# Kernel optimization log

Hardware: AMD Instinct MI355X
Metric: run time of the kernel (lower is better)

Reference implementation:

```python
import jax, jax.numpy as jnp
import numpy as np

B, L, H = 16, 2048, 1024
N = B * L
K_SEL = 8192
LN_EPS = 1e-12
PD_EPS = 1e-6  # torch f.pairwise_distance default eps


def setup_inputs() -> dict:
    key = jax.random.key(0)
    k1, k2, k3, k4 = jax.random.split(key, 4)
    msp = jax.random.normal(k1, (B, L, H), dtype=jnp.float32)
    lab = jax.random.normal(k2, (B, L, H), dtype=jnp.float32)
    # mask with exactly K_SEL true positions (static compaction size)
    perm = jax.random.permutation(k3, N)[:K_SEL]
    mask = jnp.zeros((N,), dtype=bool).at[perm].set(True).reshape(B, L)
    dense_w = jax.random.normal(k4, (H, H), dtype=jnp.float32) / np.sqrt(H)
    return {
        "masked_sentence_prediction": msp,
        "label_embeddings": lab,
        "label_mask": mask,
        "dense_w": dense_w,
        "dense_b": jnp.zeros((H,), dtype=jnp.float32),
        "ln_gamma": jnp.ones((H,), dtype=jnp.float32),
        "ln_beta": jnp.zeros((H,), dtype=jnp.float32),
        "K": K_SEL,
    }


def reference(masked_sentence_prediction, label_embeddings, label_mask,
              dense_w, dense_b, ln_gamma, ln_beta, K):
    Hd = masked_sentence_prediction.shape[-1]
    mask_flat = label_mask.reshape(-1)
    # stream compaction: rows where mask is true (static size K)
    idx = jnp.nonzero(mask_flat, size=K)[0]
    preds = masked_sentence_prediction.reshape(-1, Hd)[idx]      # [K, H]
    labels = label_embeddings.reshape(-1, Hd)[idx]               # [K, H]
    # dense + LayerNorm
    h = preds @ dense_w.T + dense_b
    mu = jnp.mean(h, axis=-1, keepdims=True)
    var = jnp.mean(jnp.square(h - mu), axis=-1, keepdims=True)
    h = (h - mu) * jax.lax.rsqrt(var + LN_EPS) * ln_gamma + ln_beta
    # contrastive logits against dynamic sentence vocabulary
    logits = h @ labels.T                                        # [K, K]
    log_probs = jax.nn.log_softmax(logits, axis=1)
    probs = jnp.exp(log_probs)
    eye = jnp.eye(K, dtype=logits.dtype)
    per_example_loss_distance = jnp.sum(jnp.abs(probs - eye + PD_EPS), axis=1)
    per_example_loss_product = -jnp.diagonal(log_probs)
    denom = K + 1e-5
    loss_distance = jnp.sum(per_example_loss_distance) / denom
    loss_product = jnp.sum(per_example_loss_product) / denom
    loss_variance_distance = jnp.var(per_example_loss_distance, ddof=1)
    loss_variance_product = jnp.var(per_example_loss_product, ddof=1)
    return (logits, per_example_loss_distance, per_example_loss_product,
            loss_distance, loss_product, loss_variance_distance, loss_variance_product)
```

## Files before the change

### kernel.cpp

```cpp
#include <hip/hip_runtime.h>
#include <cstdint>

#define NROWS 32768
#define HD    1024
#define KSEL  8192
#define LN_EPS 1e-12f
#define PD_EPS 1e-6f

typedef unsigned short u16;
typedef __bf16 bf16x8 __attribute__((ext_vector_type(8)));
typedef float  f32x4  __attribute__((ext_vector_type(4)));

__device__ inline u16 f2bf(float f) {
    union { float f; uint32_t u; } x; x.f = f;
    uint32_t r = (x.u + 0x7fffu + ((x.u >> 16) & 1u)) >> 16;
    return (u16)r;
}

__device__ inline uint2 pack4(float a, float b, float c, float d) {
    uint2 r;
    r.x = (uint32_t)f2bf(a) | ((uint32_t)f2bf(b) << 16);
    r.y = (uint32_t)f2bf(c) | ((uint32_t)f2bf(d) << 16);
    return r;
}

__global__ void compact_mask_k(const uint8_t* mb, const int32_t* mi, int* idx) {
    __shared__ int cnt[1024];
    __shared__ int tmp[1024];
    __shared__ int mode_s;
    const int t = threadIdx.x;
    const int per = NROWS / 1024;
    const int base = t * per;
    int c0 = 0;
    for (int i = 0; i < per; ++i) c0 += (mb[base + i] != 0);
    tmp[t] = c0;
    __syncthreads();
    for (int off = 512; off > 0; off >>= 1) {
        if (t < off) tmp[t] += tmp[t + off];
        __syncthreads();
    }
    if (t == 0) mode_s = (tmp[0] == KSEL) ? 0 : 1;
    __syncthreads();
    const int mode = mode_s;
    int c = c0;
    if (mode) { c = 0; for (int i = 0; i < per; ++i) c += (mi[base + i] != 0); }
    cnt[t] = c;
    __syncthreads();
    for (int off = 1; off < 1024; off <<= 1) {
        int add = (t >= off) ? cnt[t - off] : 0;
        __syncthreads();
        cnt[t] += add;
        __syncthreads();
    }
    int pos = cnt[t] - c;
    for (int i = 0; i < per; ++i) {
        bool v = mode ? (mi[base + i] != 0) : (mb[base + i] != 0);
        if (v) idx[pos++] = base + i;
    }
}

__global__ void gather_conv_k(const float* __restrict__ msp, const float* __restrict__ lab,
                              const int* __restrict__ idx, const float* __restrict__ W,
                              u16* __restrict__ predsB, u16* __restrict__ labelsB,
                              u16* __restrict__ Wb) {
    const int b = blockIdx.x;
    const int t = threadIdx.x;
    if (b < KSEL) {
        const int src = idx[b];
        float4 p = *(const float4*)(msp + (size_t)src * HD + t * 4);
        float4 q = *(const float4*)(lab + (size_t)src * HD + t * 4);
        *(uint2*)(predsB  + (size_t)b * HD + t * 4) = pack4(p.x, p.y, p.z, p.w);
        *(uint2*)(labelsB + (size_t)b * HD + t * 4) = pack4(q.x, q.y, q.z, q.w);
    } else {
        const int i = ((b - KSEL) * 256 + t) * 4;
        float4 v = *(const float4*)(W + i);
        *(uint2*)(Wb + i) = pack4(v.x, v.y, v.z, v.w);
    }
}

#define STAGE(XPTR, ROWBASE, KT, I, LBASE) do {                                      \
    const int f_ = (I) * 512 + tid;                                                  \
    const int r_ = f_ >> 3;                                                          \
    const int sp_ = (f_ & 7) ^ (r_ & 7);                                             \
    const u16* g_ = (XPTR) + (size_t)((ROWBASE) + r_) * Kd + koff + (KT) * 64 + sp_ * 8; \
    __builtin_amdgcn_global_load_lds(                                                \
        (const __attribute__((address_space(1))) void*)g_,                           \
        (__attribute__((address_space(3))) void*)(lds + (LBASE) + f_ * 8), 16, 0, 0);\
} while (0)

#define GEMM_PRO_AND_KLOOP(TVAL)                                                      \
    const int nx  = N >> 8;                                                           \
    int wg  = ((nwg & 7) == 0) ? ((bid & 7) * (nwg >> 3) + (bid >> 3)) : bid;         \
    const int bm = wg / nx, bn = wg % nx;                                             \
    const size_t brow = (size_t)bm << 8, bcol = (size_t)bn << 8;                      \
    const int tid = threadIdx.x;                                                      \
    const int l = tid & 63, wid = tid >> 6;                                           \
    const int wm = wid >> 2, wn = wid & 3;                                            \
    const int lr = l & 15, lq = l >> 4;                                               \
    const int sw = lr & 7;                                                            \
    f32x4 acc[8][4] = {};                                                             \
    const int arow = (wm * 128 + lr) * 64;                                            \
    const int brow2 = (wn * 64 + lr) * 64;                                            \
    const int s0 = (lq ^ sw) * 8;                                                     \
    const int s1 = ((4 + lq) ^ sw) * 8;                                               \
    _Pragma("unroll")                                                                 \
    for (int i = 0; i < 4; ++i) STAGE(A,  brow, 0, i, 0);                             \
    _Pragma("unroll")                                                                 \
    for (int i = 0; i < 4; ++i) STAGE(Bt, bcol, 0, i, 49152);                         \
    _Pragma("unroll")                                                                 \
    for (int i = 0; i < 4; ++i) STAGE(A,  brow, 1, i, 16384);                         \
    asm volatile("s_waitcnt vmcnt(4)" ::: "memory");                                  \
    __builtin_amdgcn_s_barrier();                                                     \
    const int T = (TVAL);                                                             \
    int abi = 0;                                                                      \
    _Pragma("unroll 1")                                                               \
    for (int t = 0; t < T; ++t) {                                                     \
        const int aB = abi * 16384;                                                   \
        const int bB = 49152 + (t & 1) * 16384;                                       \
        const int aN = (abi >= 1 ? abi - 1 : 2) * 16384;                              \
        const int bN = 49152 + ((t + 1) & 1) * 16384;                                 \
        bf16x8 a0[8], b0[4], a1[8], b1[4];                                            \
                     \
        _Pragma("unroll")                                                             \
        for (int mi = 0; mi < 8; ++mi)                                                \
            a0[mi] = *(const bf16x8*)(lds + aB + arow + mi * 1024 + s0);              \
        _Pragma("unroll")                                                             \
        for (int ni = 0; ni < 4; ++ni)                                                \
            b0[ni] = *(const bf16x8*)(lds + bB + brow2 + ni * 1024 + s0);             \
        _Pragma("unroll")                                                             \
        for (int mi = 0; mi < 8; ++mi)                                                \
            a1[mi] = *(const bf16x8*)(lds + aB + arow + mi * 1024 + s1);              \
        _Pragma("unroll")                                                             \
        for (int ni = 0; ni < 4; ++ni)                                                \
            b1[ni] = *(const bf16x8*)(lds + bB + brow2 + ni * 1024 + s1);             \
                      \
        if (t + 1 < T) {                                                              \
            STAGE(Bt, bcol, t + 1, 0, bN); STAGE(Bt, bcol, t + 1, 1, bN);             \
            STAGE(Bt, bcol, t + 1, 2, bN); STAGE(Bt, bcol, t + 1, 3, bN);             \
        }                                                                             \
        if (t + 2 < T) {                                                              \
            STAGE(A, brow, t + 2, 0, aN); STAGE(A, brow, t + 2, 1, aN);               \
            STAGE(A, brow, t + 2, 2, aN); STAGE(A, brow, t + 2, 3, aN);               \
        }                                                                             \
                     \
        _Pragma("unroll")                                                             \
        for (int mi = 0; mi < 8; ++mi) {                                              \
            _Pragma("unroll")                                                         \
            for (int ni = 0; ni < 4; ++ni)                                            \
                acc[mi][ni] = __builtin_amdgcn_mfma_f32_16x16x32_bf16(a0[mi], b0[ni], acc[mi][ni], 0, 0, 0); \
        }                                                                             \
        _Pragma("unroll")                                                             \
        for (int mi = 0; mi < 8; ++mi) {                                              \
            _Pragma("unroll")                                                         \
            for (int ni = 0; ni < 4; ++ni)                                            \
                acc[mi][ni] = __builtin_amdgcn_mfma_f32_16x16x32_bf16(a1[mi], b1[ni], acc[mi][ni], 0, 0, 0); \
        }                                                                             \
                      \
        if (t < T - 2) { asm volatile("s_waitcnt vmcnt(4)" ::: "memory"); }           \
        else           { asm volatile("s_waitcnt vmcnt(0)" ::: "memory"); }           \
        __builtin_amdgcn_s_barrier();                                                 \
        abi = (abi == 2) ? 0 : abi + 1;                                               \
    }

__global__ __launch_bounds__(512, 2)
void gemm256a_k(const u16* __restrict__ A, const u16* __restrict__ Bt,
                float* __restrict__ C, int M, int N, int Kd) {
    extern __shared__ u16 lds[];
    const int nwg = (M >> 8) * (N >> 8);
    int bid = blockIdx.x;
    const int half = (bid >= nwg) ? 1 : 0;
    if (half) bid -= nwg;
    const int KdH = Kd >> 1;
    const int koff = half * KdH;
    float* Cp = C + (size_t)half * ((size_t)M * N);
    GEMM_PRO_AND_KLOOP(KdH >> 6);
    #pragma unroll
    for (int m = 0; m < 8; ++m) {
        const size_t rb = brow + wm * 128 + m * 16 + lq * 4;
        #pragma unroll
        for (int n = 0; n < 4; ++n) {
            const size_t cb = bcol + wn * 64 + n * 16 + lr;
            #pragma unroll
            for (int rr = 0; rr < 4; ++rr)
                Cp[(rb + rr) * (size_t)N + cb] = acc[m][n][rr];
        }
    }
}

__global__ __launch_bounds__(512, 2)
void gemm256s_k(const u16* __restrict__ A, const u16* __restrict__ Bt,
                float* __restrict__ C, int M, int N, int Kd,
                float2* __restrict__ pst) {
    extern __shared__ u16 lds[];
    const int nwg = (M >> 8) * (N >> 8);
    int bid = blockIdx.x;
    const int koff = 0;
    GEMM_PRO_AND_KLOOP(Kd >> 6);

    float2* sbuf = (float2*)lds;
    #pragma unroll
    for (int m = 0; m < 8; ++m) {
        #pragma unroll
        for (int rr = 0; rr < 4; ++rr) {
            float v0 = acc[m][0][rr], v1 = acc[m][1][rr];
            float v2 = acc[m][2][rr], v3 = acc[m][3][rr];
            float mx = fmaxf(fmaxf(v0, v1), fmaxf(v2, v3));
            #pragma unroll
            for (int o = 1; o < 16; o <<= 1) mx = fmaxf(mx, __shfl_xor(mx, o));
            float se = __expf(v0 - mx) + __expf(v1 - mx) + __expf(v2 - mx) + __expf(v3 - mx);
            #pragma unroll
            for (int o = 1; o < 16; o <<= 1) se += __shfl_xor(se, o);
            if (lr == 0) {
                const int rl = wm * 128 + m * 16 + lq * 4 + rr;
                sbuf[rl * 5 + wn] = make_float2(mx, se);
            }
        }
        const size_t rb = brow + wm * 128 + m * 16 + lq * 4;
        #pragma unroll
        for (int n = 0; n < 4; ++n) {
            const size_t cb = bcol + wn * 64 + n * 16 + lr;
            #pragma unroll
            for (int rr = 0; rr < 4; ++rr)
                __builtin_nontemporal_store(acc[m][n][rr], &C[(rb + rr) * (size_t)N + cb]);
        }
    }
    asm volatile("s_waitcnt lgkmcnt(0)" ::: "memory");
    __builtin_amdgcn_s_barrier();
    if (tid < 256) {
        const float2 p0 = sbuf[tid * 5 + 0], p1 = sbuf[tid * 5 + 1];
        const float2 p2 = sbuf[tid * 5 + 2], p3 = sbuf[tid * 5 + 3];
        const float M2 = fmaxf(fmaxf(p0.x, p1.x), fmaxf(p2.x, p3.x));
        const float S2 = p0.y * __expf(p0.x - M2) + p1.y * __expf(p1.x - M2)
                       + p2.y * __expf(p2.x - M2) + p3.y * __expf(p3.x - M2);
        pst[(brow + tid) * (N >> 8) + bn] = make_float2(M2, S2);
    }
}

__global__ __launch_bounds__(256)
void loss_final_k(const float2* __restrict__ pst, const float* __restrict__ logits,
                  float* __restrict__ peld, float* __restrict__ pelp) {
    const int tid = threadIdx.x;
    const int wv = tid >> 6, half = (tid & 63) >> 5, l5 = tid & 31;
    const int row = blockIdx.x * 8 + wv * 2 + half;
    const float2 p = pst[(size_t)row * 32 + l5];
    const float d = logits[(size_t)row * (KSEL + 1)];
    float M = p.x;
    #pragma unroll
    for (int o = 1; o < 32; o <<= 1) M = fmaxf(M, __shfl_xor(M, o));
    float S = p.y * __expf(p.x - M);
    #pragma unroll
    for (int o = 1; o < 32; o <<= 1) S += __shfl_xor(S, o);
    if (l5 == 0) {
        const float pi = __expf(d - M) / S;
        peld[row] = 2.0f - 2.0f * pi + (float)(KSEL - 2) * PD_EPS;
        pelp[row] = M + __logf(S) - d;
    }
}

__device__ inline float blockSum(float v, float* red) {
    #pragma unroll
    for (int o = 32; o > 0; o >>= 1) v += __shfl_down(v, o);
    __syncthreads();
    if ((threadIdx.x & 63) == 0) red[threadIdx.x >> 6] = v;
    __syncthreads();
    return red[0] + red[1] + red[2] + red[3];
}

__global__ void ln_k(const float* __restrict__ Hp0, const float* __restrict__ Hp1,
                     const float* __restrict__ bias,
                     const float* __restrict__ gamma, const float* __restrict__ beta,
                     u16* __restrict__ Hb) {
    __shared__ float red[4];
    const int r = blockIdx.x, t = threadIdx.x;
    float4 x4 = *(const float4*)(Hp0 + (size_t)r * HD + t * 4);
    float4 y4 = *(const float4*)(Hp1 + (size_t)r * HD + t * 4);
    float4 b4 = *(const float4*)(bias + t * 4);
    float x[4] = { x4.x + y4.x + b4.x, x4.y + y4.y + b4.y,
                   x4.z + y4.z + b4.z, x4.w + y4.w + b4.w };
    float s = x[0] + x[1] + x[2] + x[3];
    float mu = blockSum(s, red) * (1.0f / HD);
    float d0 = x[0] - mu, d1 = x[1] - mu, d2 = x[2] - mu, d3 = x[3] - mu;
    float vs = d0 * d0 + d1 * d1 + d2 * d2 + d3 * d3;
    float var = blockSum(vs, red) * (1.0f / HD);
    float rs = rsqrtf(var + LN_EPS);
    float4 g4 = *(const float4*)(gamma + t * 4);
    float4 e4 = *(const float4*)(beta + t * 4);
    float y0 = d0 * rs * g4.x + e4.x;
    float y1 = d1 * rs * g4.y + e4.y;
    float y2 = d2 * rs * g4.z + e4.z;
    float y3 = d3 * rs * g4.w + e4.w;
    *(uint2*)(Hb + (size_t)r * HD + t * 4) = pack4(y0, y1, y2, y3);
}

__global__ __launch_bounds__(1024)
void reduce_k(const float* __restrict__ peld, const float* __restrict__ pelp,
              float* __restrict__ scalars) {
    __shared__ double red[4][16];
    const int t = threadIdx.x;
    double a = 0.0, b = 0.0, c = 0.0, d = 0.0;
    for (int i = t; i < KSEL; i += 1024) {
        const double pd = (double)peld[i];
        const double pp = (double)pelp[i];
        a += pd; b += pd * pd; c += pp; d += pp * pp;
    }
    #pragma unroll
    for (int o = 32; o > 0; o >>= 1) {
        a += __shfl_down(a, o); b += __shfl_down(b, o);
        c += __shfl_down(c, o); d += __shfl_down(d, o);
    }
    const int wv = t >> 6;
    if ((t & 63) == 0) { red[0][wv] = a; red[1][wv] = b; red[2][wv] = c; red[3][wv] = d; }
    __syncthreads();
    if (t == 0) {
        double s1 = 0, s2 = 0, s3 = 0, s4 = 0;
        #pragma unroll
        for (int i = 0; i < 16; ++i) { s1 += red[0][i]; s2 += red[1][i]; s3 += red[2][i]; s4 += red[3][i]; }
        const double Kd = (double)KSEL;
        const double denom = Kd + 1e-5;
        scalars[0] = (float)(s1 / denom);
        scalars[1] = (float)(s3 / denom);
        scalars[2] = (float)((s2 - s1 * s1 / Kd) / (Kd - 1.0));
        scalars[3] = (float)((s4 - s3 * s3 / Kd) / (Kd - 1.0));
    }
}

extern "C" void kernel_launch(void* const* d_in, const int* in_sizes, int n_in,
                              void* d_out, int out_size, void* d_ws, size_t ws_size,
                              hipStream_t stream) {
    const float* msp   = (const float*)d_in[0];
    const float* lab   = (const float*)d_in[1];
    const void*  mask  = d_in[2];
    const float* W     = (const float*)d_in[3];
    const float* bias  = (const float*)d_in[4];
    const float* gamma = (const float*)d_in[5];
    const float* beta  = (const float*)d_in[6];
    float* out = (float*)d_out;
    char*  ws  = (char*)d_ws;

    int*    idx     = (int*)ws;
    float2* pst     = (float2*)(ws + 65536);
    u16*    wBf     = (u16*)(ws + 65536);
    u16*    labelsB = (u16*)(ws + (size_t)(4  << 20));
    u16*    hB      = (u16*)(ws + (size_t)(20 << 20));
    u16*    predsB  = (u16*)d_out;
    float*  hPre    = out + ((size_t)8 << 20);

    float* peld    = out + (size_t)KSEL * KSEL;
    float* pelp    = peld + KSEL;
    float* scalars = pelp + KSEL;

    hipFuncSetAttribute(reinterpret_cast<const void*>(&gemm256a_k),
                        hipFuncAttributeMaxDynamicSharedMemorySize, 163840);
    hipFuncSetAttribute(reinterpret_cast<const void*>(&gemm256s_k),
                        hipFuncAttributeMaxDynamicSharedMemorySize, 163840);

    compact_mask_k<<<1, 1024, 0, stream>>>((const uint8_t*)mask, (const int32_t*)mask, idx);
    gather_conv_k<<<KSEL + 1024, 256, 0, stream>>>(msp, lab, idx, W, predsB, labelsB, wBf);
    gemm256a_k<<<2 * (KSEL / 256) * (HD / 256), 512, 163840, stream>>>(
        predsB, wBf, hPre, KSEL, HD, HD);
    ln_k<<<KSEL, 256, 0, stream>>>(hPre, hPre + (size_t)KSEL * HD, bias, gamma, beta, hB);
    gemm256s_k<<<(KSEL / 256) * (KSEL / 256), 512, 163840, stream>>>(
        hB, labelsB, out, KSEL, KSEL, HD, pst);
    loss_final_k<<<KSEL / 8, 256, 0, stream>>>(pst, out, peld, pelp);
    reduce_k<<<1, 1024, 0, stream>>>(peld, pelp, scalars);
}
```

Measured before the change: 267.2 us.

## Switch GEMM inner loop from 16x16x32 to 32x32x16 bf16 MFMA

Replaces the 16x16x32 MFMA tiling with 32x32x16 MFMA instructions. Each wave now computes 4x2 tiles of 32x32 instead of 8x4 tiles of 16x16, which changes the LDS fragment reads, the swizzle offsets and the epilogue row/column mapping. The aim is fewer MFMA issues and LDS reads per unit of work and higher matrix-core throughput. The softmax-stats epilogue now reduces across 32 lanes, and the logits store in that kernel becomes a regular store instead of a nontemporal one, which may change cache behaviour for the large logits write.

```diff
diff --git a/kernel.cpp b/kernel.cpp
--- a/kernel.cpp
+++ b/kernel.cpp
@@ -9,7 +9,7 @@
 
 typedef unsigned short u16;
 typedef __bf16 bf16x8 __attribute__((ext_vector_type(8)));
-typedef float  f32x4  __attribute__((ext_vector_type(4)));
+typedef float  f32x16 __attribute__((ext_vector_type(16)));
 
 __device__ inline u16 f2bf(float f) {
     union { float f; uint32_t u; } x; x.f = f;
@@ -96,13 +96,16 @@
     const int tid = threadIdx.x;                                                      \
     const int l = tid & 63, wid = tid >> 6;                                           \
     const int wm = wid >> 2, wn = wid & 3;                                            \
-    const int lr = l & 15, lq = l >> 4;                                               \
-    const int sw = lr & 7;                                                            \
-    f32x4 acc[8][4] = {};                                                             \
-    const int arow = (wm * 128 + lr) * 64;                                            \
-    const int brow2 = (wn * 64 + lr) * 64;                                            \
-    const int s0 = (lq ^ sw) * 8;                                                     \
-    const int s1 = ((4 + lq) ^ sw) * 8;                                               \
+    const int r5 = l & 31, hk = l >> 5;                                               \
+    const int sw = l & 7;                                                             \
+    f32x16 acc[4][2] = {};                                                            \
+    const int arow = (wm * 128 + r5) * 64;                                            \
+    const int brow2 = (wn * 64 + r5) * 64;                                            \
+                              \
+    const int s0 = ((0 + hk) ^ sw) * 8;                                               \
+    const int s1 = ((2 + hk) ^ sw) * 8;                                               \
+    const int s2 = ((4 + hk) ^ sw) * 8;                                               \
+    const int s3 = ((6 + hk) ^ sw) * 8;                                               \
     _Pragma("unroll")                                                                 \
     for (int i = 0; i < 4; ++i) STAGE(A,  brow, 0, i, 0);                             \
     _Pragma("unroll")                                                                 \
@@ -119,20 +122,22 @@
         const int bB = 49152 + (t & 1) * 16384;                                       \
         const int aN = (abi >= 1 ? abi - 1 : 2) * 16384;                              \
         const int bN = 49152 + ((t + 1) & 1) * 16384;                                 \
-        bf16x8 a0[8], b0[4], a1[8], b1[4];                                            \
-                     \
+        bf16x8 a[4][4], b[4][2];                                                      \
+                                           \
         _Pragma("unroll")                                                             \
-        for (int mi = 0; mi < 8; ++mi)                                                \
-            a0[mi] = *(const bf16x8*)(lds + aB + arow + mi * 1024 + s0);              \
+        for (int mi = 0; mi < 4; ++mi) {                                              \
+            a[0][mi] = *(const bf16x8*)(lds + aB + arow + mi * 2048 + s0);            \
+            a[1][mi] = *(const bf16x8*)(lds + aB + arow + mi * 2048 + s1);            \
+            a[2][mi] = *(const bf16x8*)(lds + aB + arow + mi * 2048 + s2);            \
+            a[3][mi] = *(const bf16x8*)(lds + aB + arow + mi * 2048 + s3);            \
+        }                                                                             \
         _Pragma("unroll")                                                             \
-        for (int ni = 0; ni < 4; ++ni)                                                \
-            b0[ni] = *(const bf16x8*)(lds + bB + brow2 + ni * 1024 + s0);             \
-        _Pragma("unroll")                                                             \
-        for (int mi = 0; mi < 8; ++mi)                                                \
-            a1[mi] = *(const bf16x8*)(lds + aB + arow + mi * 1024 + s1);              \
-        _Pragma("unroll")                                                             \
-        for (int ni = 0; ni < 4; ++ni)                                                \
-            b1[ni] = *(const bf16x8*)(lds + bB + brow2 + ni * 1024 + s1);             \
+        for (int ni = 0; ni < 2; ++ni) {                                              \
+            b[0][ni] = *(const bf16x8*)(lds + bB + brow2 + ni * 2048 + s0);           \
+            b[1][ni] = *(const bf16x8*)(lds + bB + brow2 + ni * 2048 + s1);           \
+            b[2][ni] = *(const bf16x8*)(lds + bB + brow2 + ni * 2048 + s2);           \
+            b[3][ni] = *(const bf16x8*)(lds + bB + brow2 + ni * 2048 + s3);           \
+        }                                                                             \
                       \
         if (t + 1 < T) {                                                              \
             STAGE(Bt, bcol, t + 1, 0, bN); STAGE(Bt, bcol, t + 1, 1, bN);             \
@@ -142,20 +147,17 @@
             STAGE(A, brow, t + 2, 0, aN); STAGE(A, brow, t + 2, 1, aN);               \
             STAGE(A, brow, t + 2, 2, aN); STAGE(A, brow, t + 2, 3, aN);               \
         }                                                                             \
-                     \
+              \
         _Pragma("unroll")                                                             \
-        for (int mi = 0; mi < 8; ++mi) {                                              \
+        for (int kk = 0; kk < 4; ++kk) {                                              \
             _Pragma("unroll")                                                         \
-            for (int ni = 0; ni < 4; ++ni)                                            \
-                acc[mi][ni] = __builtin_amdgcn_mfma_f32_16x16x32_bf16(a0[mi], b0[ni], acc[mi][ni], 0, 0, 0); \
-        }                                                                             \
-        _Pragma("unroll")                                                             \
-        for (int mi = 0; mi < 8; ++mi) {                                              \
-            _Pragma("unroll")                                                         \
-            for (int ni = 0; ni < 4; ++ni)                                            \
-                acc[mi][ni] = __builtin_amdgcn_mfma_f32_16x16x32_bf16(a1[mi], b1[ni], acc[mi][ni], 0, 0, 0); \
-        }                                                                             \
-                      \
+            for (int mi = 0; mi < 4; ++mi) {                                          \
+                _Pragma("unroll")                                                     \
+                for (int ni = 0; ni < 2; ++ni)                                        \
+                    acc[mi][ni] = __builtin_amdgcn_mfma_f32_32x32x16_bf16(            \
+                        a[kk][mi], b[kk][ni], acc[mi][ni], 0, 0, 0);                  \
+            }                                                                         \
+        }                                                                             \
         if (t < T - 2) { asm volatile("s_waitcnt vmcnt(4)" ::: "memory"); }           \
         else           { asm volatile("s_waitcnt vmcnt(0)" ::: "memory"); }           \
         __builtin_amdgcn_s_barrier();                                                 \
@@ -175,14 +177,16 @@
     float* Cp = C + (size_t)half * ((size_t)M * N);
     GEMM_PRO_AND_KLOOP(KdH >> 6);
     #pragma unroll
-    for (int m = 0; m < 8; ++m) {
-        const size_t rb = brow + wm * 128 + m * 16 + lq * 4;
+    for (int mi = 0; mi < 4; ++mi) {
         #pragma unroll
-        for (int n = 0; n < 4; ++n) {
-            const size_t cb = bcol + wn * 64 + n * 16 + lr;
+        for (int ni = 0; ni < 2; ++ni) {
+            const size_t cb = bcol + wn * 64 + ni * 32 + r5;
             #pragma unroll
-            for (int rr = 0; rr < 4; ++rr)
-                Cp[(rb + rr) * (size_t)N + cb] = acc[m][n][rr];
+            for (int reg = 0; reg < 16; ++reg) {
+                const size_t rb = brow + wm * 128 + mi * 32
+                                + (reg & 3) + 8 * (reg >> 2) + 4 * hk;
+                Cp[rb * (size_t)N + cb] = acc[mi][ni][reg];
+            }
         }
     }
 }
@@ -199,29 +203,30 @@
 
     float2* sbuf = (float2*)lds;
     #pragma unroll
-    for (int m = 0; m < 8; ++m) {
+    for (int mi = 0; mi < 4; ++mi) {
         #pragma unroll
-        for (int rr = 0; rr < 4; ++rr) {
-            float v0 = acc[m][0][rr], v1 = acc[m][1][rr];
-            float v2 = acc[m][2][rr], v3 = acc[m][3][rr];
-            float mx = fmaxf(fmaxf(v0, v1), fmaxf(v2, v3));
+        for (int reg = 0; reg < 16; ++reg) {
+            const float v0 = acc[mi][0][reg], v1 = acc[mi][1][reg];
+            float mx = fmaxf(v0, v1);
             #pragma unroll
-            for (int o = 1; o < 16; o <<= 1) mx = fmaxf(mx, __shfl_xor(mx, o));
-            float se = __expf(v0 - mx) + __expf(v1 - mx) + __expf(v2 - mx) + __expf(v3 - mx);
+            for (int o = 1; o < 32; o <<= 1) mx = fmaxf(mx, __shfl_xor(mx, o));
+            float se = __expf(v0 - mx) + __expf(v1 - mx);
             #pragma unroll
-            for (int o = 1; o < 16; o <<= 1) se += __shfl_xor(se, o);
-            if (lr == 0) {
-                const int rl = wm * 128 + m * 16 + lq * 4 + rr;
+            for (int o = 1; o < 32; o <<= 1) se += __shfl_xor(se, o);
+            if (r5 == 0) {
+                const int rl = wm * 128 + mi * 32 + (reg & 3) + 8 * (reg >> 2) + 4 * hk;
                 sbuf[rl * 5 + wn] = make_float2(mx, se);
             }
         }
-        const size_t rb = brow + wm * 128 + m * 16 + lq * 4;
         #pragma unroll
-        for (int n = 0; n < 4; ++n) {
-            const size_t cb = bcol + wn * 64 + n * 16 + lr;
+        for (int ni = 0; ni < 2; ++ni) {
+            const size_t cb = bcol + wn * 64 + ni * 32 + r5;
             #pragma unroll
-            for (int rr = 0; rr < 4; ++rr)
-                __builtin_nontemporal_store(acc[m][n][rr], &C[(rb + rr) * (size_t)N + cb]);
+            for (int reg = 0; reg < 16; ++reg) {
+                const size_t rb = brow + wm * 128 + mi * 32
+                                + (reg & 3) + 8 * (reg >> 2) + 4 * hk;
+                C[rb * (size_t)N + cb] = acc[mi][ni][reg];
+            }
         }
     }
     asm volatile("s_waitcnt lgkmcnt(0)" ::: "memory");
```

New measurement: 335.5 us. 25.5% more time.
